# Kernel tuning notes

Hardware: AMD Instinct MI355X
Metric: run time of the kernel (lower is better)

Reference implementation:

```python
import jax, jax.numpy as jnp
import numpy as np

B, T, C, H = 2, 2048, 1024, 16
D = C // H  # head_dim = 64

def setup_inputs() -> dict:
    key = jax.random.key(0)
    k1, k2, k3 = jax.random.split(key, 3)
    x = jax.random.normal(k1, (B, T, C), dtype=jnp.float32)
    W_attn = jax.random.normal(k2, (C, 3 * C), dtype=jnp.float32) * (1.0 / np.sqrt(C))
    W_proj = jax.random.normal(k3, (C, C), dtype=jnp.float32) * (1.0 / np.sqrt(C))
    return {"x": x, "W_attn": W_attn, "W_proj": W_proj}

def reference(x, W_attn, W_proj):
    b, t, c = x.shape
    qkv = x @ W_attn                       # [B,T,3C]
    q, k, v = jnp.split(qkv, 3, axis=-1)
    # [B,T,C] -> [B,H,T,D]
    q = q.reshape(b, t, H, D).transpose(0, 2, 1, 3)
    k = k.reshape(b, t, H, D).transpose(0, 2, 1, 3)
    v = v.reshape(b, t, H, D).transpose(0, 2, 1, 3)
    scale = 1.0 / np.sqrt(D).astype(np.float32)
    att = jnp.einsum('bhqd,bhkd->bhqk', q, k) * scale   # [B,H,T,T]
    causal = jnp.tril(jnp.ones((t, t), dtype=bool))
    att = jnp.where(causal[None, None], att, -jnp.inf)
    att = jax.nn.softmax(att, axis=-1)
    y = jnp.einsum('bhqk,bhkd->bhqd', att, v)           # [B,H,T,D]
    y = y.transpose(0, 2, 1, 3).reshape(b, t, c)        # [B,T,C]
    return y @ W_proj
```

## Files before the change

### kernel.cpp

```cpp
#include <hip/hip_runtime.h>
#include <hip/hip_bf16.h>
#include <cstdint>
#include <cstddef>
#include <cmath>

typedef __attribute__((ext_vector_type(8))) short short8v;
typedef __attribute__((ext_vector_type(4))) float f32x4;
typedef __attribute__((ext_vector_type(4))) unsigned short ushort4v;

__device__ __forceinline__ unsigned short f2bf(float f) {
  union { float f; uint32_t u; } v; v.f = f;
  uint32_t u = v.u;
  return (unsigned short)((u + 0x7fffu + ((u >> 16) & 1u)) >> 16);
}

__device__ __forceinline__ float bf2f(unsigned short u) {
  union { uint32_t u; float f; } v; v.u = ((uint32_t)u) << 16; return v.f;
}

__device__ __forceinline__ uint32_t pack2bf(float a, float b) {
  __hip_bfloat162 h = __float22bfloat162_rn(make_float2(a, b));
  union { __hip_bfloat162 h; uint32_t u; } c; c.h = h; return c.u;
}

__device__ __forceinline__ void load_lds_16B(const void* g, void* l) {
  __builtin_amdgcn_global_load_lds((const __attribute__((address_space(1))) void*)g,
                                   (__attribute__((address_space(3))) void*)l, 16, 0, 0);
}

__global__ __launch_bounds__(256) void prep_kernel(const float* __restrict__ x,
                                                   unsigned short* __restrict__ xb,
                                                   const float* __restrict__ Wa,
                                                   unsigned short* __restrict__ WaT,
                                                   const float* __restrict__ Wp,
                                                   unsigned short* __restrict__ WpT) {
  __shared__ float tile[64][65];
  int bid = blockIdx.x;
  int tid = threadIdx.x;

  if (bid < 2048) {
    int i = bid * 256 + tid;
    const float4* s4 = (const float4*)x + (size_t)i * 2;
    float4 f0 = s4[0], f1 = s4[1];
    short8v o;
    o[0] = (short)f2bf(f0.x); o[1] = (short)f2bf(f0.y);
    o[2] = (short)f2bf(f0.z); o[3] = (short)f2bf(f0.w);
    o[4] = (short)f2bf(f1.x); o[5] = (short)f2bf(f1.y);
    o[6] = (short)f2bf(f1.z); o[7] = (short)f2bf(f1.w);
    *(short8v*)(xb + (size_t)i * 8) = o;
    return;
  }

  int t = bid - 2048;
  const float* W; unsigned short* WT; int N, n0, k0;
  if (t < 768) { W = Wa; WT = WaT; N = 3072; n0 = (t % 48) * 64; k0 = (t / 48) * 64; }
  else { t -= 768; W = Wp; WT = WpT; N = 1024; n0 = (t % 16) * 64; k0 = (t / 16) * 64; }
  const int K = 1024;

#pragma unroll
  for (int i = 0; i < 4; ++i) {
    int idx = i * 256 + tid;
    int r = idx >> 4, c4 = (idx & 15) * 4;
    float4 v = *(const float4*)(W + (size_t)(k0 + r) * N + n0 + c4);
    tile[r][c4] = v.x; tile[r][c4 + 1] = v.y; tile[r][c4 + 2] = v.z; tile[r][c4 + 3] = v.w;
  }
  __syncthreads();
#pragma unroll
  for (int i = 0; i < 4; ++i) {
    int idx = i * 256 + tid;
    int nr = idx >> 4, k4 = (idx & 15) * 4;
    ushort4 o;
    o.x = f2bf(tile[k4 + 0][nr]);
    o.y = f2bf(tile[k4 + 1][nr]);
    o.z = f2bf(tile[k4 + 2][nr]);
    o.w = f2bf(tile[k4 + 3][nr]);
    *(ushort4*)(WT + (size_t)(n0 + nr) * K + k0 + k4) = o;
  }
}

__global__ __launch_bounds__(256) void gemm_qkv_kernel(const unsigned short* __restrict__ A,
                                                       const unsigned short* __restrict__ BT,
                                                       unsigned short* __restrict__ qk,
                                                       unsigned short* __restrict__ VT) {
  const int K = 1024, N = 3072;
  __shared__ __align__(16) char lds[32768];
  char* As = lds;
  char* Bs = lds + 16384;

  int nbn = N >> 7;
  int nwg = gridDim.x;
  int wg = blockIdx.x;
  int per = nwg >> 3;
  int swz = (wg & 7) * per + (wg >> 3);
  int tm = swz / nbn, tn = swz % nbn;

  int tid = threadIdx.x;
  int wid = tid >> 6, lane = tid & 63;
  int l15 = lane & 15, lhi = lane >> 4;
  int wm = wid >> 1, wn = wid & 1;

  const unsigned short* Abase = A + (size_t)(tm * 128) * K;
  const unsigned short* Bbase = BT + (size_t)(tn * 128) * K;

  size_t ofs[4];
#pragma unroll
  for (int i = 0; i < 4; ++i) {
    int row = i * 32 + (tid >> 3);
    int ss = (tid & 7) ^ (row & 7);
    ofs[i] = (size_t)row * K + ss * 8;
  }

  f32x4 acc[4][4] = {};

  for (int kt = 0; kt < K; kt += 64) {
    __syncthreads();
#pragma unroll
    for (int i = 0; i < 4; ++i)
      load_lds_16B(Abase + ofs[i] + kt, As + i * 4096 + tid * 16);
#pragma unroll
    for (int i = 0; i < 4; ++i)
      load_lds_16B(Bbase + ofs[i] + kt, Bs + i * 4096 + tid * 16);
    __syncthreads();

#pragma unroll
    for (int ks = 0; ks < 2; ++ks) {
      short8v af[4], bfr[4];
#pragma unroll
      for (int mi = 0; mi < 4; ++mi) {
        int row = wm * 64 + mi * 16 + l15;
        int ss = (ks * 4 + lhi) ^ (row & 7);
        af[mi] = *(const short8v*)(As + row * 128 + ss * 16);
      }
#pragma unroll
      for (int ni = 0; ni < 4; ++ni) {
        int row = wn * 64 + ni * 16 + l15;
        int ss = (ks * 4 + lhi) ^ (row & 7);
        bfr[ni] = *(const short8v*)(Bs + row * 128 + ss * 16);
      }
#pragma unroll
      for (int mi = 0; mi < 4; ++mi)
#pragma unroll
        for (int ni = 0; ni < 4; ++ni)
          acc[mi][ni] = __builtin_amdgcn_mfma_f32_16x16x32_bf16(af[mi], bfr[ni], acc[mi][ni], 0, 0, 0);
    }
  }

#pragma unroll
  for (int mi = 0; mi < 4; ++mi)
#pragma unroll
    for (int ni = 0; ni < 4; ++ni) {
      int col = tn * 128 + wn * 64 + ni * 16 + l15;
      int row0 = tm * 128 + wm * 64 + mi * 16 + lhi * 4;
      if (col < 2048) {
#pragma unroll
        for (int r = 0; r < 4; ++r)
          qk[(size_t)(row0 + r) * 2048 + col] = f2bf(acc[mi][ni][r]);
      } else {
        int hl = col - 2048, hh = hl >> 6, d = hl & 63;
        int bb = row0 >> 11, tl = row0 & 2047;
        int tc = tl >> 6, k = (tl & 63) >> 2;
        int c4 = ((k >> 3) << 5) | ((k & 3) << 3) | (k & 4);
        ushort4 w;
        w.x = f2bf(acc[mi][ni][0]); w.y = f2bf(acc[mi][ni][1]);
        w.z = f2bf(acc[mi][ni][2]); w.w = f2bf(acc[mi][ni][3]);
        *(ushort4*)(VT + ((size_t)((bb * 16 + hh) * 64 + d)) * 2048 + tc * 64 + c4) = w;
      }
    }
}

__global__ __launch_bounds__(256) void gemm_bt64_kernel(const unsigned short* __restrict__ A,
                                                        const unsigned short* __restrict__ BT,
                                                        float* __restrict__ Cout,
                                                        int M, int N, int K) {
  __shared__ __align__(16) char lds[24576];
  char* As = lds;
  char* Bs = lds + 8192;

  int nbn = N >> 7;
  int nwg = gridDim.x;
  int wg = blockIdx.x;
  int per = nwg >> 3;
  int swz = (wg & 7) * per + (wg >> 3);
  int tm = swz / nbn, tn = swz % nbn;

  int tid = threadIdx.x;
  int wid = tid >> 6, lane = tid & 63;
  int l15 = lane & 15, lhi = lane >> 4;

  const unsigned short* Abase = A + (size_t)(tm * 64) * K;
  const unsigned short* Bbase = BT + (size_t)(tn * 128) * K;

  size_t ofsA[2], ofsB[4];
#pragma unroll
  for (int i = 0; i < 2; ++i) {
    int row = i * 32 + (tid >> 3);
    int ss = (tid & 7) ^ (row & 7);
    ofsA[i] = (size_t)row * K + ss * 8;
  }
#pragma unroll
  for (int i = 0; i < 4; ++i) {
    int row = i * 32 + (tid >> 3);
    int ss = (tid & 7) ^ (row & 7);
    ofsB[i] = (size_t)row * K + ss * 8;
  }

  f32x4 acc[4][2] = {};

  for (int kt = 0; kt < K; kt += 64) {
    __syncthreads();
#pragma unroll
    for (int i = 0; i < 2; ++i)
      load_lds_16B(Abase + ofsA[i] + kt, As + i * 4096 + tid * 16);
#pragma unroll
    for (int i = 0; i < 4; ++i)
      load_lds_16B(Bbase + ofsB[i] + kt, Bs + i * 4096 + tid * 16);
    __syncthreads();

#pragma unroll
    for (int ks = 0; ks < 2; ++ks) {
      short8v af[4], bfr[2];
#pragma unroll
      for (int mi = 0; mi < 4; ++mi) {
        int row = mi * 16 + l15;
        int ss = (ks * 4 + lhi) ^ (row & 7);
        af[mi] = *(const short8v*)(As + row * 128 + ss * 16);
      }
#pragma unroll
      for (int ni = 0; ni < 2; ++ni) {
        int row = wid * 32 + ni * 16 + l15;
        int ss = (ks * 4 + lhi) ^ (row & 7);
        bfr[ni] = *(const short8v*)(Bs + row * 128 + ss * 16);
      }
#pragma unroll
      for (int mi = 0; mi < 4; ++mi)
#pragma unroll
        for (int ni = 0; ni < 2; ++ni)
          acc[mi][ni] = __builtin_amdgcn_mfma_f32_16x16x32_bf16(af[mi], bfr[ni], acc[mi][ni], 0, 0, 0);
    }
  }

#pragma unroll
  for (int mi = 0; mi < 4; ++mi)
#pragma unroll
    for (int ni = 0; ni < 2; ++ni)
#pragma unroll
      for (int r = 0; r < 4; ++r) {
        int row = tm * 64 + mi * 16 + lhi * 4 + r;
        int col = tn * 128 + wid * 32 + ni * 16 + l15;
        Cout[(size_t)row * N + col] = acc[mi][ni][r];
      }
}

__device__ __forceinline__ short8v scale_q(short8v q) {
  short8v r;
#pragma unroll
  for (int j = 0; j < 8; ++j)
    r[j] = (short)f2bf(bf2f((unsigned short)q[j]) * 0.18033688f);
  return r;
}

__device__ __forceinline__ void mask_diag(f32x4 s[4], int q_abs, int k0, int lhi) {
#pragma unroll
  for (int ni = 0; ni < 4; ++ni)
#pragma unroll
    for (int r = 0; r < 4; ++r) {
      int kv = k0 + ni * 16 + lhi * 4 + r;
      if (kv > q_abs) s[ni][r] = -1e30f;
    }
}

__device__ __forceinline__ void exp_p(f32x4 s[4]) {
#pragma unroll
  for (int ni = 0; ni < 4; ++ni)
#pragma unroll
    for (int r = 0; r < 4; ++r)
      s[ni][r] = exp2f(s[ni][r]);
}

__device__ __forceinline__ void repack_pa(const f32x4 s[4], short8v pa[2]) {
#pragma unroll
  for (int ks = 0; ks < 2; ++ks) {
    union { uint32_t u[4]; short8v v; } pk;
    pk.u[0] = pack2bf(s[2 * ks][0], s[2 * ks][1]);
    pk.u[1] = pack2bf(s[2 * ks][2], s[2 * ks][3]);
    pk.u[2] = pack2bf(s[2 * ks + 1][0], s[2 * ks + 1][1]);
    pk.u[3] = pack2bf(s[2 * ks + 1][2], s[2 * ks + 1][3]);
    pa[ks] = pk.v;
  }
}

__global__ __launch_bounds__(256) void attn_kernel(const unsigned short* __restrict__ qk,
                                                   const unsigned short* __restrict__ VT,
                                                   unsigned short* __restrict__ yb) {
  const int T = 2048, LD = 2048;
  int bid = blockIdx.x;
  int qt = 31 - (bid >> 5);
  int bh = bid & 31;
  int b = bh >> 4, h = bh & 15;

  int tid = threadIdx.x;
  int wid = tid >> 6, lane = tid & 63;
  int l15 = lane & 15, lhi = lane >> 4;

  __shared__ __align__(16) char Ks[2][8192];
  __shared__ __align__(16) char Vt[2][8192];

  union { uint32_t u[4]; short8v v; } ob;
  ob.u[0] = ob.u[1] = ob.u[2] = ob.u[3] = 0x3F803F80u;
  const short8v onesv = ob.v;

  int qrow = qt * 64 + wid * 16 + l15;
  const unsigned short* qp = qk + (size_t)(b * T + qrow) * LD + h * 64;
  short8v qf[2];
  qf[0] = scale_q(*(const short8v*)(qp + lhi * 8));
  qf[1] = scale_q(*(const short8v*)(qp + 32 + lhi * 8));

  const unsigned short* kbase = qk + (size_t)b * T * LD + 1024 + h * 64;
  const unsigned short* vtbase = VT + (size_t)(b * 16 + h) * 64 * 2048;

  f32x4 o[4] = {};
  f32x4 lf = {};
  int q_abs = qrow;
  int nt = qt + 1;

  auto stageK = [&](int s) {
#pragma unroll
    for (int i2 = 0; i2 < 2; ++i2) {
      int row = i2 * 32 + (tid >> 3);
      int ss = (tid & 7) ^ (row & 7);
      load_lds_16B(kbase + (size_t)(s * 64 + row) * LD + ss * 8, Ks[s & 1] + i2 * 4096 + tid * 16);
    }
  };
  auto stageV = [&](int s) {
#pragma unroll
    for (int i2 = 0; i2 < 2; ++i2) {
      int row = i2 * 32 + (tid >> 3);
      int ss = (tid & 7) ^ (row & 7);
      load_lds_16B(vtbase + (size_t)row * 2048 + s * 64 + ss * 8, Vt[s & 1] + i2 * 4096 + tid * 16);
    }
  };

  stageK(0); stageV(0);
  __syncthreads();

  for (int s = 0; s < nt; ++s) {
    if (s + 1 < nt) { stageK(s + 1); stageV(s + 1); }

    const char* KC = Ks[s & 1];
    const char* VC = Vt[s & 1];
    int k0 = s * 64;

    f32x4 sv[4] = {};
    __builtin_amdgcn_s_setprio(1);
#pragma unroll
    for (int ks = 0; ks < 2; ++ks)
#pragma unroll
      for (int ni = 0; ni < 4; ++ni) {
        int row = ni * 16 + l15;
        int sl = (ks * 4 + lhi) ^ (row & 7);
        short8v kf = *(const short8v*)(KC + row * 128 + sl * 16);
        sv[ni] = __builtin_amdgcn_mfma_f32_16x16x32_bf16(kf, qf[ks], sv[ni], 0, 0, 0);
      }
    __builtin_amdgcn_s_setprio(0);

    if (s == qt) mask_diag(sv, q_abs, k0, lhi);
    exp_p(sv);

    short8v pa[2];
    repack_pa(sv, pa);

    __builtin_amdgcn_s_setprio(1);
#pragma unroll
    for (int ks = 0; ks < 2; ++ks) {
#pragma unroll
      for (int nd = 0; nd < 4; ++nd) {
        int d = nd * 16 + l15;
        int slv = (ks * 4 + lhi) ^ (d & 7);
        short8v bv = *(const short8v*)(VC + d * 128 + slv * 16);
        o[nd] = __builtin_amdgcn_mfma_f32_16x16x32_bf16(pa[ks], bv, o[nd], 0, 0, 0);
      }
      lf = __builtin_amdgcn_mfma_f32_16x16x32_bf16(pa[ks], onesv, lf, 0, 0, 0);
    }
    __builtin_amdgcn_s_setprio(0);

    __syncthreads();
  }

#pragma unroll
  for (int r = 0; r < 4; ++r) {
    float inv = 1.0f / lf[r];
    int q = qt * 64 + wid * 16 + lhi * 4 + r;
#pragma unroll
    for (int nd = 0; nd < 4; ++nd)
      yb[(size_t)(b * T + q) * 1024 + h * 64 + nd * 16 + l15] = f2bf(o[nd][r] * inv);
  }
}

extern "C" void kernel_launch(void* const* d_in, const int* in_sizes, int n_in,
                              void* d_out, int out_size, void* d_ws, size_t ws_size,
                              hipStream_t stream) {
  const float* x = (const float*)d_in[0];
  const float* Wa = (const float*)d_in[1];
  const float* Wp = (const float*)d_in[2];
  float* out = (float*)d_out;

  char* ws = (char*)d_ws;
  unsigned short* xb  = (unsigned short*)(ws);
  unsigned short* WaT = (unsigned short*)(ws + (size_t)(8u  << 20));
  unsigned short* WpT = (unsigned short*)(ws + (size_t)(14u << 20));
  unsigned short* qk  = (unsigned short*)(ws + (size_t)(16u << 20));
  unsigned short* VT  = (unsigned short*)(ws + (size_t)(32u << 20));
  unsigned short* yb  = (unsigned short*)(ws + (size_t)(40u << 20));

  prep_kernel<<<dim3(3072), 256, 0, stream>>>(x, xb, Wa, WaT, Wp, WpT);
  gemm_qkv_kernel<<<dim3(768), 256, 0, stream>>>(xb, WaT, qk, VT);
  attn_kernel<<<dim3(1024), 256, 0, stream>>>(qk, VT, yb);
  gemm_bt64_kernel<<<dim3(512), 256, 0, stream>>>(yb, WpT, out, 4096, 1024, 1024);
}
```

Measured before the change: 99.94 us.

## Process two adjacent query tiles per attention block to reuse K/V tiles

Each attention block now handles two consecutive 64-row query tiles (qlo, qhi) and shares every staged K/V tile between them, halving the grid to 512 blocks. This reduces redundant K/V loads from global memory into LDS and amortizes the staging and barrier cost over twice the MFMA work. It raises register pressure with doubled accumulators and keeps causal imbalance across blocks, and the lower tile sits idle on its final step.

```diff
diff --git a/kernel.cpp b/kernel.cpp
--- a/kernel.cpp
+++ b/kernel.cpp
@@ -251,6 +251,7 @@
       }
 }
 
+
 __device__ __forceinline__ short8v scale_q(short8v q) {
   short8v r;
 #pragma unroll
@@ -294,9 +295,10 @@
                                                    unsigned short* __restrict__ yb) {
   const int T = 2048, LD = 2048;
   int bid = blockIdx.x;
-  int qt = 31 - (bid >> 5);
+  int c = 15 - (bid >> 5);
   int bh = bid & 31;
   int b = bh >> 4, h = bh & 15;
+  int qlo = 2 * c, qhi = 2 * c + 1;
 
   int tid = threadIdx.x;
   int wid = tid >> 6, lane = tid & 63;
@@ -309,19 +311,22 @@
   ob.u[0] = ob.u[1] = ob.u[2] = ob.u[3] = 0x3F803F80u;
   const short8v onesv = ob.v;
 
-  int qrow = qt * 64 + wid * 16 + l15;
-  const unsigned short* qp = qk + (size_t)(b * T + qrow) * LD + h * 64;
-  short8v qf[2];
-  qf[0] = scale_q(*(const short8v*)(qp + lhi * 8));
-  qf[1] = scale_q(*(const short8v*)(qp + 32 + lhi * 8));
+  int qrowL = qlo * 64 + wid * 16 + l15;
+  int qrowH = qhi * 64 + wid * 16 + l15;
+  const unsigned short* qpL = qk + (size_t)(b * T + qrowL) * LD + h * 64;
+  const unsigned short* qpH = qk + (size_t)(b * T + qrowH) * LD + h * 64;
+  short8v qfL[2], qfH[2];
+  qfL[0] = scale_q(*(const short8v*)(qpL + lhi * 8));
+  qfL[1] = scale_q(*(const short8v*)(qpL + 32 + lhi * 8));
+  qfH[0] = scale_q(*(const short8v*)(qpH + lhi * 8));
+  qfH[1] = scale_q(*(const short8v*)(qpH + 32 + lhi * 8));
 
   const unsigned short* kbase = qk + (size_t)b * T * LD + 1024 + h * 64;
   const unsigned short* vtbase = VT + (size_t)(b * 16 + h) * 64 * 2048;
 
-  f32x4 o[4] = {};
-  f32x4 lf = {};
-  int q_abs = qrow;
-  int nt = qt + 1;
+  f32x4 oL[4] = {}, oH[4] = {};
+  f32x4 lfL = {}, lfH = {};
+  int nt = qhi + 1;
 
   auto stageK = [&](int s) {
 #pragma unroll
@@ -349,8 +354,9 @@
     const char* KC = Ks[s & 1];
     const char* VC = Vt[s & 1];
     int k0 = s * 64;
-
-    f32x4 sv[4] = {};
+    bool actL = s <= qlo;
+
+    f32x4 sH[4] = {}, sL[4] = {};
     __builtin_amdgcn_s_setprio(1);
 #pragma unroll
     for (int ks = 0; ks < 2; ++ks)
@@ -359,15 +365,21 @@
         int row = ni * 16 + l15;
         int sl = (ks * 4 + lhi) ^ (row & 7);
         short8v kf = *(const short8v*)(KC + row * 128 + sl * 16);
-        sv[ni] = __builtin_amdgcn_mfma_f32_16x16x32_bf16(kf, qf[ks], sv[ni], 0, 0, 0);
+        sH[ni] = __builtin_amdgcn_mfma_f32_16x16x32_bf16(kf, qfH[ks], sH[ni], 0, 0, 0);
+        if (actL) sL[ni] = __builtin_amdgcn_mfma_f32_16x16x32_bf16(kf, qfL[ks], sL[ni], 0, 0, 0);
       }
     __builtin_amdgcn_s_setprio(0);
 
-    if (s == qt) mask_diag(sv, q_abs, k0, lhi);
-    exp_p(sv);
-
-    short8v pa[2];
-    repack_pa(sv, pa);
+    if (s == qhi) mask_diag(sH, qrowH, k0, lhi);
+    exp_p(sH);
+    if (actL) {
+      if (s == qlo) mask_diag(sL, qrowL, k0, lhi);
+      exp_p(sL);
+    }
+
+    short8v paH[2], paL[2];
+    repack_pa(sH, paH);
+    if (actL) repack_pa(sL, paL);
 
     __builtin_amdgcn_s_setprio(1);
 #pragma unroll
@@ -377,9 +389,11 @@
         int d = nd * 16 + l15;
         int slv = (ks * 4 + lhi) ^ (d & 7);
         short8v bv = *(const short8v*)(VC + d * 128 + slv * 16);
-        o[nd] = __builtin_amdgcn_mfma_f32_16x16x32_bf16(pa[ks], bv, o[nd], 0, 0, 0);
-      }
-      lf = __builtin_amdgcn_mfma_f32_16x16x32_bf16(pa[ks], onesv, lf, 0, 0, 0);
+        oH[nd] = __builtin_amdgcn_mfma_f32_16x16x32_bf16(paH[ks], bv, oH[nd], 0, 0, 0);
+        if (actL) oL[nd] = __builtin_amdgcn_mfma_f32_16x16x32_bf16(paL[ks], bv, oL[nd], 0, 0, 0);
+      }
+      lfH = __builtin_amdgcn_mfma_f32_16x16x32_bf16(paH[ks], onesv, lfH, 0, 0, 0);
+      if (actL) lfL = __builtin_amdgcn_mfma_f32_16x16x32_bf16(paL[ks], onesv, lfL, 0, 0, 0);
     }
     __builtin_amdgcn_s_setprio(0);
 
@@ -388,11 +402,15 @@
 
 #pragma unroll
   for (int r = 0; r < 4; ++r) {
-    float inv = 1.0f / lf[r];
-    int q = qt * 64 + wid * 16 + lhi * 4 + r;
-#pragma unroll
-    for (int nd = 0; nd < 4; ++nd)
-      yb[(size_t)(b * T + q) * 1024 + h * 64 + nd * 16 + l15] = f2bf(o[nd][r] * inv);
+    float invH = 1.0f / lfH[r];
+    float invL = 1.0f / lfL[r];
+    int qH = qhi * 64 + wid * 16 + lhi * 4 + r;
+    int qL = qlo * 64 + wid * 16 + lhi * 4 + r;
+#pragma unroll
+    for (int nd = 0; nd < 4; ++nd) {
+      yb[(size_t)(b * T + qH) * 1024 + h * 64 + nd * 16 + l15] = f2bf(oH[nd][r] * invH);
+      yb[(size_t)(b * T + qL) * 1024 + h * 64 + nd * 16 + l15] = f2bf(oL[nd][r] * invL);
+    }
   }
 }
 
@@ -414,6 +432,6 @@
 
   prep_kernel<<<dim3(3072), 256, 0, stream>>>(x, xb, Wa, WaT, Wp, WpT);
   gemm_qkv_kernel<<<dim3(768), 256, 0, stream>>>(xb, WaT, qk, VT);
-  attn_kernel<<<dim3(1024), 256, 0, stream>>>(qk, VT, yb);
+  attn_kernel<<<dim3(512), 256, 0, stream>>>(qk, VT, yb);
   gemm_bt64_kernel<<<dim3(512), 256, 0, stream>>>(yb, WpT, out, 4096, 1024, 1024);
 }
```

Result: slower. 137.4 us (+37.4%).
